# Optimization experiments

Measured on AMD Instinct MI355X. Metric: run time of the kernel, lower is better.

The kernel has to match this reference:

```python
import jax, jax.numpy as jnp
import numpy as np

N_NODES = 50000
N_EDGES = 800000
IN_DIM = 128
OUT_DIM = 128


def setup_inputs() -> dict:
    key = jax.random.key(0)
    k_h, k_w, k_src, k_dst = jax.random.split(key, 4)
    h = jax.random.normal(k_h, (N_NODES, IN_DIM), dtype=jnp.float32)
    # xavier-uniform weight
    limit = float(np.sqrt(6.0 / (IN_DIM + OUT_DIM)))
    W = jax.random.uniform(k_w, (IN_DIM, OUT_DIM), dtype=jnp.float32,
                           minval=-limit, maxval=limit)
    b = jnp.zeros((OUT_DIM,), dtype=jnp.float32)
    src = jax.random.randint(k_src, (N_EDGES,), 0, N_NODES, dtype=jnp.int64)
    dst = jax.random.randint(k_dst, (N_EDGES,), 0, N_NODES, dtype=jnp.int64)
    # GCN symmetric norm: deg^{-1/2} based on in-degree (clamped to >=1)
    deg = jax.ops.segment_sum(jnp.ones((N_EDGES,), jnp.float32), dst,
                              num_segments=N_NODES)
    norm = (jnp.maximum(deg, 1.0) ** -0.5)[:, None]  # [N,1]
    return {"h": h, "norm": norm, "W": W, "b": b, "src": src, "dst": dst}


def reference(h, norm, W, b, src, dst):
    # dense projection: [N, in] @ [in, out]
    h = h @ W
    # pre-aggregation norm scale
    h = h * norm
    # copy_src + sum: gather source features, segment-sum into destination nodes
    msgs = h[src]  # [E, out]
    h = jax.ops.segment_sum(msgs, dst, num_segments=h.shape[0])
    # post-aggregation norm scale + bias
    h = h * norm + b
    return h
```

## Files before the change

### kernel.cpp

```cpp
#include <hip/hip_runtime.h>

#define N_NODES 50000
#define N_EDGES 800000
#define SCAN_NB 49

#define NBUCKETS 196
#define BIN_EDGES 4096
#define BIN_NB 196
#define BUCKET_CAP 5120

#define GEMM_NB ((N_NODES + 63) / 64)
#define FUSED_NB 980

typedef __attribute__((ext_vector_type(4))) _Float16 half4;
typedef __attribute__((ext_vector_type(8))) _Float16 half8;
typedef __attribute__((ext_vector_type(4))) float f32x4;

__device__ __forceinline__ int deg_from_norm(float n)
{
    return __float2int_rn(1.0f / (n * n));
}

__global__ __launch_bounds__(256) void prep_wt_kernel(
    const float* __restrict__ W, _Float16* __restrict__ Wt)
{
    const int e = blockIdx.x * 256 + threadIdx.x;
    const int c = e & 127;
    const int k4 = (e >> 7) << 2;
    half4 v;
    v.x = (_Float16)W[(k4 + 0) * 128 + c];
    v.y = (_Float16)W[(k4 + 1) * 128 + c];
    v.z = (_Float16)W[(k4 + 2) * 128 + c];
    v.w = (_Float16)W[(k4 + 3) * 128 + c];
    *(half4*)(Wt + (size_t)c * 128 + k4) = v;
}

__global__ __launch_bounds__(256) void fused_gemm_bin_kernel(
    const float* __restrict__ h, const float* __restrict__ norm,
    const _Float16* __restrict__ Wt, _Float16* __restrict__ t,
    const int* __restrict__ src, const int* __restrict__ dst,
    int* __restrict__ bcur, int2* __restrict__ bucketbuf)
{
    const int tid = threadIdx.x;
    const int bid = blockIdx.x;

    if (bid % 5 == 4) {
        __shared__ int hist[NBUCKETS];
        const int bs = (bid / 5) * BIN_EDGES;
        for (int i = tid; i < NBUCKETS; i += 256) hist[i] = 0;
        __syncthreads();
#pragma unroll
        for (int j = 0; j < 4; ++j) {
            int e4 = bs + (j * 256 + tid) * 4;
            if (e4 < N_EDGES) {
                int4 d4 = *(const int4*)(dst + e4);
                atomicAdd(&hist[d4.x >> 8], 1);
                atomicAdd(&hist[d4.y >> 8], 1);
                atomicAdd(&hist[d4.z >> 8], 1);
                atomicAdd(&hist[d4.w >> 8], 1);
            }
        }
        __syncthreads();
        int base = 0;
        if (tid < NBUCKETS) {
            int hc = hist[tid];
            if (hc) base = atomicAdd(&bcur[tid], hc);
        }
        __syncthreads();
        if (tid < NBUCKETS) hist[tid] = base;
        __syncthreads();
#pragma unroll
        for (int j = 0; j < 4; ++j) {
            int e4 = bs + (j * 256 + tid) * 4;
            if (e4 < N_EDGES) {
                int4 d4 = *(const int4*)(dst + e4);
                int4 s4 = *(const int4*)(src + e4);
                int b0, p;
                b0 = d4.x >> 8; p = atomicAdd(&hist[b0], 1);
                bucketbuf[(size_t)b0 * BUCKET_CAP + p] = make_int2(s4.x, d4.x);
                b0 = d4.y >> 8; p = atomicAdd(&hist[b0], 1);
                bucketbuf[(size_t)b0 * BUCKET_CAP + p] = make_int2(s4.y, d4.y);
                b0 = d4.z >> 8; p = atomicAdd(&hist[b0], 1);
                bucketbuf[(size_t)b0 * BUCKET_CAP + p] = make_int2(s4.z, d4.z);
                b0 = d4.w >> 8; p = atomicAdd(&hist[b0], 1);
                bucketbuf[(size_t)b0 * BUCKET_CAP + p] = make_int2(s4.w, d4.w);
            }
        }
        return;
    }

    __shared__ __align__(16) _Float16 WtS[128 * 136];
    __shared__ __align__(16) _Float16 HhS[64 * 136];
    __shared__ float norms[64];
    const int gemm_id = bid - bid / 5;
    if (gemm_id >= GEMM_NB) return;
    const int rbase = gemm_id * 64;

#pragma unroll
    for (int i = 0; i < 8; ++i) {
        int f = i * 256 + tid;
        int c = f >> 4;
        int k8 = (f & 15) << 3;
        *(half8*)(WtS + c * 136 + k8) = *(const half8*)(Wt + (size_t)c * 128 + k8);
    }
#pragma unroll
    for (int i = 0; i < 8; ++i) {
        int f = i * 256 + tid;
        int row = f >> 5;
        int c4 = (f & 31) << 2;
        int gr = rbase + row;
        float4 v = make_float4(0.f, 0.f, 0.f, 0.f);
        if (gr < N_NODES) v = *(const float4*)(h + (size_t)gr * 128 + c4);
        half4 hv;
        hv.x = (_Float16)v.x; hv.y = (_Float16)v.y;
        hv.z = (_Float16)v.z; hv.w = (_Float16)v.w;
        *(half4*)(HhS + row * 136 + c4) = hv;
    }
    if (tid < 64) {
        int gr = rbase + tid;
        norms[tid] = (gr < N_NODES) ? norm[gr] : 0.f;
    }
    __syncthreads();

    const int wid = tid >> 6, lane = tid & 63;
    const int lrow = lane & 15;
    const int lk = (lane >> 4) << 3;
    const int r0 = wid * 16;

    half8 a[4];
#pragma unroll
    for (int ks = 0; ks < 4; ++ks)
        a[ks] = *(const half8*)(HhS + (r0 + lrow) * 136 + ks * 32 + lk);

    const int rq = r0 + ((lane >> 4) << 2);
    float nv[4];
#pragma unroll
    for (int reg = 0; reg < 4; ++reg) nv[reg] = norms[rq + reg];

#pragma unroll
    for (int ct = 0; ct < 8; ++ct) {
        const int c0 = ct * 16;
        f32x4 acc = {0.f, 0.f, 0.f, 0.f};
#pragma unroll
        for (int ks = 0; ks < 4; ++ks) {
            half8 bf = *(const half8*)(WtS + (c0 + lrow) * 136 + ks * 32 + lk);
            acc = __builtin_amdgcn_mfma_f32_16x16x32_f16(a[ks], bf, acc, 0, 0, 0);
        }
#pragma unroll
        for (int reg = 0; reg < 4; ++reg) {
            int gr = rbase + rq + reg;
            if (gr < N_NODES)
                t[(size_t)gr * 128 + c0 + lrow] = (_Float16)(acc[reg] * nv[reg]);
        }
    }
}

__global__ __launch_bounds__(256) void scan_sums_kernel(
    const float* __restrict__ norm, int* __restrict__ bsum,
    int* __restrict__ bcur)
{
    const int tid = threadIdx.x;
    if (blockIdx.x == 0 && tid < NBUCKETS) bcur[tid] = 0;
    const int idx = blockIdx.x * 1024 + tid * 4;
    int s = 0;
    if (idx < N_NODES) {
        float4 n = *(const float4*)(norm + idx);
        s = deg_from_norm(n.x) + deg_from_norm(n.y) +
            deg_from_norm(n.z) + deg_from_norm(n.w);
    }
#pragma unroll
    for (int d = 32; d > 0; d >>= 1) s += __shfl_down(s, d);
    __shared__ int ws[4];
    if ((tid & 63) == 0) ws[tid >> 6] = s;
    __syncthreads();
    if (tid == 0) bsum[blockIdx.x] = ws[0] + ws[1] + ws[2] + ws[3];
}

__global__ __launch_bounds__(64) void scan_bsum_kernel(
    const int* __restrict__ bsum, int* __restrict__ boff)
{
    const int tid = threadIdx.x;
    int v = (tid < SCAN_NB) ? bsum[tid] : 0;
    int inc = v;
#pragma unroll
    for (int d = 1; d < 64; d <<= 1) {
        int u = __shfl_up(inc, d);
        if (tid >= d) inc += u;
    }
    if (tid < SCAN_NB) boff[tid] = inc - v;
}

__global__ __launch_bounds__(256) void scan_write_kernel(
    const float* __restrict__ norm, const int* __restrict__ boff,
    int* __restrict__ off)
{
    const int tid = threadIdx.x;
    const int idx = blockIdx.x * 1024 + tid * 4;

    int4 v = make_int4(0, 0, 0, 0);
    if (idx < N_NODES) {
        float4 n = *(const float4*)(norm + idx);
        v.x = deg_from_norm(n.x); v.y = deg_from_norm(n.y);
        v.z = deg_from_norm(n.z); v.w = deg_from_norm(n.w);
    }
    const int s = v.x + v.y + v.z + v.w;

    const int lane = tid & 63, w = tid >> 6;
    int inc = s;
#pragma unroll
    for (int d = 1; d < 64; d <<= 1) {
        int u = __shfl_up(inc, d);
        if (lane >= d) inc += u;
    }
    __shared__ int wsum[4];
    if (lane == 63) wsum[w] = inc;
    __syncthreads();
    int woff = 0;
    for (int i = 0; i < w; ++i) woff += wsum[i];

    int o0 = boff[blockIdx.x] + woff + inc - s;
    int o1 = o0 + v.x;
    int o2 = o1 + v.y;
    int o3 = o2 + v.z;

    if (idx < N_NODES) {
        *(int4*)(off + idx) = make_int4(o0, o1, o2, o3);
    }
}

__global__ __launch_bounds__(256) void scatter_kernel(
    const int2* __restrict__ bucketbuf, const int* __restrict__ bcur,
    const int* __restrict__ off, int* __restrict__ cur,
    int* __restrict__ esrc)
{
    const int tid = threadIdx.x;
    const int b = blockIdx.x;
    __shared__ int lcur[256];
    const int g = b * 256 + tid;
    lcur[tid] = (g < N_NODES) ? off[g] : 0;
    __syncthreads();

    const int n = bcur[b];
    const int2* buf = bucketbuf + (size_t)b * BUCKET_CAP;
    for (int i = tid; i < n; i += 256) {
        int2 p = buf[i];
        int pos = atomicAdd(&lcur[p.y & 255], 1);
        esrc[pos] = p.x;
    }
    __syncthreads();
    if (g < N_NODES) cur[g] = lcur[tid];
}

__global__ __launch_bounds__(256) void aggregate_kernel(
    const int* __restrict__ off, const int* __restrict__ cur,
    const int* __restrict__ esrc, const _Float16* __restrict__ t,
    const float* __restrict__ norm, const float* __restrict__ b,
    float* __restrict__ out)
{
    const int g = blockIdx.x * 16 + (threadIdx.x >> 4);
    if (g >= N_NODES) return;
    const int l = threadIdx.x & 15;
    const int c = l << 3;
    const int i0 = off[g], i1 = cur[g];

    float acc0[8], acc1[8];
#pragma unroll
    for (int j = 0; j < 8; ++j) { acc0[j] = 0.f; acc1[j] = 0.f; }

    int i = i0;
    for (; i + 2 <= i1; i += 2) {
        int s0 = esrc[i];
        int s1 = esrc[i + 1];
        half8 v0 = *(const half8*)(t + (size_t)s0 * 128 + c);
        half8 v1 = *(const half8*)(t + (size_t)s1 * 128 + c);
#pragma unroll
        for (int j = 0; j < 8; ++j) { acc0[j] += (float)v0[j]; acc1[j] += (float)v1[j]; }
    }
    if (i < i1) {
        int s0 = esrc[i];
        half8 v0 = *(const half8*)(t + (size_t)s0 * 128 + c);
#pragma unroll
        for (int j = 0; j < 8; ++j) acc0[j] += (float)v0[j];
    }

    const float nv = norm[g];
    const float4 b0 = *(const float4*)(b + c);
    const float4 b1 = *(const float4*)(b + c + 4);
    float4 o0 = make_float4((acc0[0] + acc1[0]) * nv + b0.x,
                            (acc0[1] + acc1[1]) * nv + b0.y,
                            (acc0[2] + acc1[2]) * nv + b0.z,
                            (acc0[3] + acc1[3]) * nv + b0.w);
    float4 o1 = make_float4((acc0[4] + acc1[4]) * nv + b1.x,
                            (acc0[5] + acc1[5]) * nv + b1.y,
                            (acc0[6] + acc1[6]) * nv + b1.z,
                            (acc0[7] + acc1[7]) * nv + b1.w);
    *(float4*)(out + (size_t)g * 128 + c) = o0;
    *(float4*)(out + (size_t)g * 128 + c + 4) = o1;
}

static inline size_t align256(size_t x) { return (x + 255) & ~(size_t)255; }

extern "C" void kernel_launch(void* const* d_in, const int* in_sizes, int n_in,
                              void* d_out, int out_size, void* d_ws, size_t ws_size,
                              hipStream_t stream)
{
    const float* h    = (const float*)d_in[0];
    const float* norm = (const float*)d_in[1];
    const float* W    = (const float*)d_in[2];
    const float* b    = (const float*)d_in[3];
    const int*   src  = (const int*)d_in[4];
    const int*   dst  = (const int*)d_in[5];
    float* out = (float*)d_out;

    char* ws = (char*)d_ws;
    size_t o = 0;
    _Float16* t = (_Float16*)(ws + o);  o = align256(o + (size_t)N_NODES * 128 * 2);
    _Float16* Wt = (_Float16*)(ws + o); o = align256(o + (size_t)128 * 128 * 2);
    int* off = (int*)(ws + o);          o = align256(o + (size_t)N_NODES * 4);
    int* cur = (int*)(ws + o);          o = align256(o + (size_t)N_NODES * 4);
    int* esrc = (int*)(ws + o);         o = align256(o + ((size_t)N_EDGES + 1024) * 4);
    int* bsum = (int*)(ws + o);         o = align256(o + (size_t)SCAN_NB * 4);
    int* boff = (int*)(ws + o);         o = align256(o + (size_t)SCAN_NB * 4);
    int* bcur = (int*)(ws + o);         o = align256(o + (size_t)NBUCKETS * 4);
    int2* bucketbuf = (int2*)(ws + o);  o = align256(o + (size_t)NBUCKETS * BUCKET_CAP * 8);

    prep_wt_kernel<<<16, 256, 0, stream>>>(W, Wt);
    scan_sums_kernel<<<SCAN_NB, 256, 0, stream>>>(norm, bsum, bcur);
    scan_bsum_kernel<<<1, 64, 0, stream>>>(bsum, boff);
    scan_write_kernel<<<SCAN_NB, 256, 0, stream>>>(norm, boff, off);
    fused_gemm_bin_kernel<<<FUSED_NB, 256, 0, stream>>>(h, norm, Wt, t,
                                                        src, dst, bcur, bucketbuf);
    scatter_kernel<<<NBUCKETS, 256, 0, stream>>>(bucketbuf, bcur, off, cur, esrc);
    aggregate_kernel<<<(N_NODES + 15) / 16, 256, 0, stream>>>(off, cur, esrc, t, norm, b, out);
}
```

Baseline: 74.84 us.

## Halve bucket width and load GEMM operands directly from global memory

Buckets for the CSR build now cover 128 destination nodes instead of 256. That doubles the bucket count and gives the scatter kernel more blocks with a smaller shared cursor array. The fused GEMM blocks no longer stage W and h tiles in LDS. Each lane loads its A fragment straight from h and its B fragment from Wt in global memory, removing the LDS staging and barrier. In exchange, Wt reads are repeated per wave and rely on the cache, and the scatter launch count must match the new bucket count, which is not shown.

```diff
diff --git a/kernel.cpp b/kernel.cpp
--- a/kernel.cpp
+++ b/kernel.cpp
@@ -4,10 +4,10 @@
 #define N_EDGES 800000
 #define SCAN_NB 49
 
-#define NBUCKETS 196
+#define NBUCKETS 391
 #define BIN_EDGES 4096
 #define BIN_NB 196
-#define BUCKET_CAP 5120
+#define BUCKET_CAP 2560
 
 #define GEMM_NB ((N_NODES + 63) / 64)
 #define FUSED_NB 980
@@ -54,20 +54,17 @@
             int e4 = bs + (j * 256 + tid) * 4;
             if (e4 < N_EDGES) {
                 int4 d4 = *(const int4*)(dst + e4);
-                atomicAdd(&hist[d4.x >> 8], 1);
-                atomicAdd(&hist[d4.y >> 8], 1);
-                atomicAdd(&hist[d4.z >> 8], 1);
-                atomicAdd(&hist[d4.w >> 8], 1);
+                atomicAdd(&hist[d4.x >> 7], 1);
+                atomicAdd(&hist[d4.y >> 7], 1);
+                atomicAdd(&hist[d4.z >> 7], 1);
+                atomicAdd(&hist[d4.w >> 7], 1);
             }
         }
         __syncthreads();
-        int base = 0;
-        if (tid < NBUCKETS) {
-            int hc = hist[tid];
-            if (hc) base = atomicAdd(&bcur[tid], hc);
-        }
-        __syncthreads();
-        if (tid < NBUCKETS) hist[tid] = base;
+        for (int i = tid; i < NBUCKETS; i += 256) {
+            int hc = hist[i];
+            hist[i] = hc ? atomicAdd(&bcur[i], hc) : 0;
+        }
         __syncthreads();
 #pragma unroll
         for (int j = 0; j < 4; ++j) {
@@ -76,66 +73,52 @@
                 int4 d4 = *(const int4*)(dst + e4);
                 int4 s4 = *(const int4*)(src + e4);
                 int b0, p;
-                b0 = d4.x >> 8; p = atomicAdd(&hist[b0], 1);
+                b0 = d4.x >> 7; p = atomicAdd(&hist[b0], 1);
                 bucketbuf[(size_t)b0 * BUCKET_CAP + p] = make_int2(s4.x, d4.x);
-                b0 = d4.y >> 8; p = atomicAdd(&hist[b0], 1);
+                b0 = d4.y >> 7; p = atomicAdd(&hist[b0], 1);
                 bucketbuf[(size_t)b0 * BUCKET_CAP + p] = make_int2(s4.y, d4.y);
-                b0 = d4.z >> 8; p = atomicAdd(&hist[b0], 1);
+                b0 = d4.z >> 7; p = atomicAdd(&hist[b0], 1);
                 bucketbuf[(size_t)b0 * BUCKET_CAP + p] = make_int2(s4.z, d4.z);
-                b0 = d4.w >> 8; p = atomicAdd(&hist[b0], 1);
+                b0 = d4.w >> 7; p = atomicAdd(&hist[b0], 1);
                 bucketbuf[(size_t)b0 * BUCKET_CAP + p] = make_int2(s4.w, d4.w);
             }
         }
         return;
     }
 
-    __shared__ __align__(16) _Float16 WtS[128 * 136];
-    __shared__ __align__(16) _Float16 HhS[64 * 136];
-    __shared__ float norms[64];
     const int gemm_id = bid - bid / 5;
     if (gemm_id >= GEMM_NB) return;
     const int rbase = gemm_id * 64;
 
-#pragma unroll
-    for (int i = 0; i < 8; ++i) {
-        int f = i * 256 + tid;
-        int c = f >> 4;
-        int k8 = (f & 15) << 3;
-        *(half8*)(WtS + c * 136 + k8) = *(const half8*)(Wt + (size_t)c * 128 + k8);
-    }
-#pragma unroll
-    for (int i = 0; i < 8; ++i) {
-        int f = i * 256 + tid;
-        int row = f >> 5;
-        int c4 = (f & 31) << 2;
-        int gr = rbase + row;
-        float4 v = make_float4(0.f, 0.f, 0.f, 0.f);
-        if (gr < N_NODES) v = *(const float4*)(h + (size_t)gr * 128 + c4);
-        half4 hv;
-        hv.x = (_Float16)v.x; hv.y = (_Float16)v.y;
-        hv.z = (_Float16)v.z; hv.w = (_Float16)v.w;
-        *(half4*)(HhS + row * 136 + c4) = hv;
-    }
-    if (tid < 64) {
-        int gr = rbase + tid;
-        norms[tid] = (gr < N_NODES) ? norm[gr] : 0.f;
-    }
-    __syncthreads();
-
     const int wid = tid >> 6, lane = tid & 63;
     const int lrow = lane & 15;
-    const int lk = (lane >> 4) << 3;
+    const int khi = (lane >> 4) << 3;
     const int r0 = wid * 16;
+    const int gr = rbase + r0 + lrow;
 
     half8 a[4];
 #pragma unroll
-    for (int ks = 0; ks < 4; ++ks)
-        a[ks] = *(const half8*)(HhS + (r0 + lrow) * 136 + ks * 32 + lk);
-
-    const int rq = r0 + ((lane >> 4) << 2);
+    for (int ks = 0; ks < 4; ++ks) {
+        float4 f0 = make_float4(0.f, 0.f, 0.f, 0.f);
+        float4 f1 = f0;
+        if (gr < N_NODES) {
+            const float* hp = h + (size_t)gr * 128 + ks * 32 + khi;
+            f0 = *(const float4*)hp;
+            f1 = *(const float4*)(hp + 4);
+        }
+        half8 av;
+        av[0] = (_Float16)f0.x; av[1] = (_Float16)f0.y;
+        av[2] = (_Float16)f0.z; av[3] = (_Float16)f0.w;
+        av[4] = (_Float16)f1.x; av[5] = (_Float16)f1.y;
+        av[6] = (_Float16)f1.z; av[7] = (_Float16)f1.w;
+        a[ks] = av;
+    }
+
+    const int rq = rbase + r0 + ((lane >> 4) << 2);
     float nv[4];
 #pragma unroll
-    for (int reg = 0; reg < 4; ++reg) nv[reg] = norms[rq + reg];
+    for (int reg = 0; reg < 4; ++reg)
+        nv[reg] = (rq + reg < N_NODES) ? norm[rq + reg] : 0.f;
 
 #pragma unroll
     for (int ct = 0; ct < 8; ++ct) {
@@ -143,14 +126,13 @@
         f32x4 acc = {0.f, 0.f, 0.f, 0.f};
 #pragma unroll
         for (int ks = 0; ks < 4; ++ks) {
-            half8 bf = *(const half8*)(WtS + (c0 + lrow) * 136 + ks * 32 + lk);
+            half8 bf = *(const half8*)(Wt + (size_t)(c0 + lrow) * 128 + ks * 32 + khi);
             acc = __builtin_amdgcn_mfma_f32_16x16x32_f16(a[ks], bf, acc, 0, 0, 0);
         }
 #pragma unroll
         for (int reg = 0; reg < 4; ++reg) {
-            int gr = rbase + rq + reg;
-            if (gr < N_NODES)
-                t[(size_t)gr * 128 + c0 + lrow] = (_Float16)(acc[reg] * nv[reg]);
+            if (rq + reg < N_NODES)
+                t[(size_t)(rq + reg) * 128 + c0 + lrow] = (_Float16)(acc[reg] * nv[reg]);
         }
     }
 }
@@ -160,7 +142,9 @@
     int* __restrict__ bcur)
 {
     const int tid = threadIdx.x;
-    if (blockIdx.x == 0 && tid < NBUCKETS) bcur[tid] = 0;
+    if (blockIdx.x == 0) {
+        for (int i = tid; i < NBUCKETS; i += 256) bcur[i] = 0;
+    }
     const int idx = blockIdx.x * 1024 + tid * 4;
     int s = 0;
     if (idx < N_NODES) {
@@ -235,20 +219,20 @@
 {
     const int tid = threadIdx.x;
     const int b = blockIdx.x;
-    __shared__ int lcur[256];
-    const int g = b * 256 + tid;
-    lcur[tid] = (g < N_NODES) ? off[g] : 0;
+    __shared__ int lcur[128];
+    const int g = b * 128 + tid;
+    if (tid < 128) lcur[tid] = (g < N_NODES) ? off[g] : 0;
     __syncthreads();
 
     const int n = bcur[b];
     const int2* buf = bucketbuf + (size_t)b * BUCKET_CAP;
     for (int i = tid; i < n; i += 256) {
         int2 p = buf[i];
-        int pos = atomicAdd(&lcur[p.y & 255], 1);
+        int pos = atomicAdd(&lcur[p.y & 127], 1);
         esrc[pos] = p.x;
     }
     __syncthreads();
-    if (g < N_NODES) cur[g] = lcur[tid];
+    if (tid < 128 && g < N_NODES) cur[g] = lcur[tid];
 }
 
 __global__ __launch_bounds__(256) void aggregate_kernel(
```

Result: slower. 78.53 us (+4.9%).
